# Kernel optimization log

Measured on AMD Instinct MI355X. Metric: run time of the kernel, lower is better.

## Reference

```python
import jax, jax.numpy as jnp
import numpy as np

B, T, H = 32, 2048, 1024

def setup_inputs() -> dict:
    key = jax.random.key(0)
    ks = jax.random.split(key, 8)
    s = 1.0 / np.sqrt(H)
    return {
        "query": jax.random.normal(ks[0], (B, H), dtype=jnp.float32),
        "values": jax.random.normal(ks[1], (B, T, H), dtype=jnp.float32),
        "Wq": jax.random.uniform(ks[2], (H, H), jnp.float32, -s, s),
        "bq": jax.random.uniform(ks[3], (H,), jnp.float32, -s, s),
        "Wv": jax.random.uniform(ks[4], (H, H), jnp.float32, -s, s),
        "bv": jax.random.uniform(ks[5], (H,), jnp.float32, -s, s),
        "Vw": jax.random.uniform(ks[6], (1, H), jnp.float32, -s, s),
        "Vb": jax.random.uniform(ks[7], (1,), jnp.float32, -s, s),
    }

def reference(query, values, Wq, bq, Wv, bv, Vw, Vb):
    # q_proj: [B,1,H], v_proj: [B,T,H]
    q_proj = (query @ Wq.T + bq)[:, None, :]
    v_proj = jnp.einsum('bth,oh->bto', values, Wv) + bv
    # score: [B,T,1] = tanh(...) @ Vw.T + Vb
    score = jnp.einsum('bth,oh->bto', jnp.tanh(q_proj + v_proj), Vw) + Vb
    attention_weights = jax.nn.softmax(score, axis=1)  # over time
    context_vector = jnp.sum(attention_weights * values, axis=1)  # [B,H]
    return (context_vector, attention_weights)
```

## Files before the change

### kernel.cpp

```cpp
#include <hip/hip_runtime.h>

#define BATCH 32
#define TT    2048
#define HH    1024
#define MTOT  (BATCH * TT)

typedef unsigned short ushort_t;
typedef short sh8 __attribute__((ext_vector_type(8)));
typedef float f4 __attribute__((ext_vector_type(4)));
typedef unsigned short us8 __attribute__((ext_vector_type(8)));

__device__ __forceinline__ ushort_t f2bf(float f) {
    unsigned u = __float_as_uint(f);
    u = (u + 0x7fffu + ((u >> 16) & 1u)) >> 16;
    return (ushort_t)u;
}
__device__ __forceinline__ float bf2f(ushort_t h) {
    return __uint_as_float(((unsigned)h) << 16);
}
__device__ __forceinline__ float fast_tanh(float x) {
    float e = __expf(2.0f * x);
    return 1.0f - 2.0f * __builtin_amdgcn_rcpf(e + 1.0f);
}

__device__ __forceinline__ void glds16(const void* g, void* l) {
    __builtin_amdgcn_global_load_lds(
        (const __attribute__((address_space(1))) void*)g,
        (__attribute__((address_space(3))) void*)l, 16, 0, 0);
}

__global__ void cvt_bf16_k(const float* __restrict__ in, ushort_t* __restrict__ out, long n) {
    long i = ((long)blockIdx.x * blockDim.x + threadIdx.x) * 8;
    if (i + 8 > n) return;
    float4 a = *(const float4*)(in + i);
    float4 b = *(const float4*)(in + i + 4);
    us8 o;
    o[0]=f2bf(a.x); o[1]=f2bf(a.y); o[2]=f2bf(a.z); o[3]=f2bf(a.w);
    o[4]=f2bf(b.x); o[5]=f2bf(b.y); o[6]=f2bf(b.z); o[7]=f2bf(b.w);
    *(us8*)(out + i) = o;
}

__global__ void qproj_k(const float* __restrict__ query, const float* __restrict__ Wq,
                        const float* __restrict__ bq, const float* __restrict__ bv,
                        float* __restrict__ qp) {
    int o = blockIdx.x, tid = threadIdx.x;
    float4 w4 = *(const float4*)(Wq + (long)o * HH + tid * 4);
    __shared__ float sm[BATCH][4];
    int wid = tid >> 6, lane = tid & 63;
    for (int b = 0; b < BATCH; ++b) {
        float4 q4 = *(const float4*)(query + (long)b * HH + tid * 4);
        float p = q4.x*w4.x + q4.y*w4.y + q4.z*w4.z + q4.w*w4.w;
        #pragma unroll
        for (int m = 1; m < 64; m <<= 1) p += __shfl_xor(p, m);
        if (lane == 0) sm[b][wid] = p;
    }
    __syncthreads();
    if (tid < BATCH) {
        float s = sm[tid][0] + sm[tid][1] + sm[tid][2] + sm[tid][3] + bq[o] + bv[o];
        qp[(long)tid * HH + o] = s;
    }
}


#define PBAR()  __builtin_amdgcn_s_barrier()
#define LGKM0() asm volatile("s_waitcnt lgkmcnt(0)" ::: "memory")
#define VMW(n)  asm volatile("s_waitcnt vmcnt(" #n ")" ::: "memory")
#define PRIO(p) __builtin_amdgcn_s_setprio(p)

__device__ __forceinline__ void stage_half(const ushort_t* __restrict__ gbase,
                                           long row0, int kb,
                                           char* ldsbase, int h, int w8, int lane) {
    #pragma unroll
    for (int c = 0; c < 2; ++c) {
        int r  = h * 128 + c * 64 + w8 + (lane >> 3);
        int sg = (lane & 7) ^ (r & 7);
        glds16(gbase + (row0 + r) * (long)HH + kb + sg * 8,
               ldsbase + (h * 128 + c * 64 + w8) * 128);
    }
}

#define READ_A(Lp, ibase)                                                        \
    { _Pragma("unroll") for (int i2_ = 0; i2_ < 4; ++i2_) {                      \
        int r_ = wr * 128 + ((ibase) + i2_) * 16 + l16;                          \
        _Pragma("unroll") for (int kq_ = 0; kq_ < 2; ++kq_)                      \
            af[i2_][kq_] = *(const sh8*)((Lp) + r_ * 128 +                       \
                                          ((((kq_ * 4) + quad) ^ (r_ & 7)) * 16)); } }

#define READ_B(Lp, jbase)                                                        \
    { _Pragma("unroll") for (int j2_ = 0; j2_ < 2; ++j2_) {                      \
        int r_ = wc * 64 + ((jbase) + j2_) * 16 + l16;                           \
        _Pragma("unroll") for (int kq_ = 0; kq_ < 2; ++kq_)                      \
            bf[(jbase) + j2_][kq_] = *(const sh8*)((Lp) + r_ * 128 +             \
                                          ((((kq_ * 4) + quad) ^ (r_ & 7)) * 16)); } }

#define MFMA_Q(ibase, jbase)                                                     \
    { _Pragma("unroll") for (int kq_ = 0; kq_ < 2; ++kq_) {                      \
      _Pragma("unroll") for (int i2_ = 0; i2_ < 4; ++i2_) {                      \
      _Pragma("unroll") for (int j2_ = 0; j2_ < 2; ++j2_) {                      \
            acc[(ibase) + i2_][(jbase) + j2_] =                                  \
                __builtin_amdgcn_mfma_f32_16x16x32_bf16(                         \
                    af[i2_][kq_], bf[(jbase) + j2_][kq_],                        \
                    acc[(ibase) + i2_][(jbase) + j2_], 0, 0, 0); } } } }

__global__ __launch_bounds__(512, 2) void score_gemm_k(
    const ushort_t* __restrict__ A, const ushort_t* __restrict__ Bw,
    const float* __restrict__ qp, const float* __restrict__ Vw,
    float* __restrict__ score)
{
    __shared__ ushort_t As[2][256 * 64];
    __shared__ ushort_t Bs[2][256 * 64];
    const int tid  = threadIdx.x;
    const int w    = tid >> 6, lane = tid & 63;
    const int quad = lane >> 4, l16 = lane & 15;
    const int wr   = w >> 2, wc = w & 3;
    const int w8   = w << 3;

    int bx   = blockIdx.x;
    int wgid = (bx & 7) * 128 + (bx >> 3);
    int mt   = wgid >> 2, nt = wgid & 3;
    const long m0 = (long)mt * 256;
    const long n0 = (long)nt * 256;

    char* As0 = (char*)&As[0][0];
    char* As1 = (char*)&As[1][0];
    char* Bs0 = (char*)&Bs[0][0];
    char* Bs1 = (char*)&Bs[1][0];

    f4  acc[8][4] = {};
    sh8 af[4][2], bf[4][2];

    stage_half(A,  m0, 0,  As0, 0, w8, lane);
    stage_half(A,  m0, 0,  As0, 1, w8, lane);
    stage_half(Bw, n0, 0,  Bs0, 0, w8, lane);
    stage_half(Bw, n0, 0,  Bs0, 1, w8, lane);
    stage_half(Bw, n0, 64, Bs1, 0, w8, lane);
    stage_half(Bw, n0, 64, Bs1, 1, w8, lane);
    VMW(4); PBAR();

    for (int it = 0; it < 7; ++it) {
        const int kb1 = (2 * it + 1) * 64;
        const int kb2 = (2 * it + 2) * 64;
        const int kb3 = (2 * it + 3) * 64;
        READ_A(As0, 0); READ_B(Bs0, 0);
        stage_half(A, m0, kb1, As1, 0, w8, lane);
        PBAR(); LGKM0(); PRIO(1); MFMA_Q(0, 0); PRIO(0); PBAR();
        READ_B(Bs0, 2);
        stage_half(A, m0, kb1, As1, 1, w8, lane);
        PBAR(); LGKM0(); PRIO(1); MFMA_Q(0, 2); PRIO(0); PBAR();
        READ_A(As0, 4);
        stage_half(Bw, n0, kb2, Bs0, 0, w8, lane);
        PBAR(); LGKM0(); PRIO(1); MFMA_Q(4, 2); PRIO(0); PBAR();
        stage_half(Bw, n0, kb2, Bs0, 1, w8, lane);
        VMW(4); PBAR(); PRIO(1); MFMA_Q(4, 0); PRIO(0); PBAR();
        READ_A(As1, 0); READ_B(Bs1, 0);
        stage_half(A, m0, kb2, As0, 0, w8, lane);
        PBAR(); LGKM0(); PRIO(1); MFMA_Q(0, 0); PRIO(0); PBAR();
        READ_B(Bs1, 2);
        stage_half(A, m0, kb2, As0, 1, w8, lane);
        PBAR(); LGKM0(); PRIO(1); MFMA_Q(0, 2); PRIO(0); PBAR();
        READ_A(As1, 4);
        stage_half(Bw, n0, kb3, Bs1, 0, w8, lane);
        PBAR(); LGKM0(); PRIO(1); MFMA_Q(4, 2); PRIO(0); PBAR();
        stage_half(Bw, n0, kb3, Bs1, 1, w8, lane);
        VMW(4); PBAR(); PRIO(1); MFMA_Q(4, 0); PRIO(0); PBAR();
    }
    {
        const int kb1 = 15 * 64;
        READ_A(As0, 0); READ_B(Bs0, 0);
        stage_half(A, m0, kb1, As1, 0, w8, lane);
        PBAR(); LGKM0(); PRIO(1); MFMA_Q(0, 0); PRIO(0); PBAR();
        READ_B(Bs0, 2);
        stage_half(A, m0, kb1, As1, 1, w8, lane);
        PBAR(); LGKM0(); PRIO(1); MFMA_Q(0, 2); PRIO(0); PBAR();
        READ_A(As0, 4);
        PBAR(); LGKM0(); PRIO(1); MFMA_Q(4, 2); PRIO(0); PBAR();
        VMW(0); PBAR(); PRIO(1); MFMA_Q(4, 0); PRIO(0); PBAR();
        READ_A(As1, 0); READ_B(Bs1, 0);
        PBAR(); LGKM0(); PRIO(1); MFMA_Q(0, 0); PRIO(0); PBAR();
        READ_B(Bs1, 2);
        PBAR(); LGKM0(); PRIO(1); MFMA_Q(0, 2); PRIO(0); PBAR();
        READ_A(As1, 4);
        PBAR(); LGKM0(); PRIO(1); MFMA_Q(4, 2); MFMA_Q(4, 0); PRIO(0);
    }

    int bidx = (int)(m0 >> 11);
    const float* qpb = qp + (long)bidx * HH;
    float qv[4], vw[4];
    #pragma unroll
    for (int j = 0; j < 4; ++j) {
        int cg = (int)n0 + wc * 64 + j * 16 + l16;
        qv[j] = qpb[cg];
        vw[j] = Vw[cg];
    }
    #pragma unroll
    for (int i = 0; i < 8; ++i) {
        #pragma unroll
        for (int r = 0; r < 4; ++r) {
            float sum = 0.0f;
            #pragma unroll
            for (int j = 0; j < 4; ++j) {
                float xv = acc[i][j][r] + qv[j];
                sum += fast_tanh(xv) * vw[j];
            }
            sum += __shfl_xor(sum, 1);
            sum += __shfl_xor(sum, 2);
            sum += __shfl_xor(sum, 4);
            sum += __shfl_xor(sum, 8);
            if (l16 == 0) {
                atomicAdd(score + m0 + wr * 128 + i * 16 + quad * 4 + r, sum);
            }
        }
    }
}

__global__ void softmax_k(const float* __restrict__ sc, float* __restrict__ w) {
    int b = blockIdx.x, tid = threadIdx.x;
    const float* s = sc + (long)b * TT;
    float v[8];
    float4 a0 = *(const float4*)(s + tid * 8);
    float4 a1 = *(const float4*)(s + tid * 8 + 4);
    v[0]=a0.x; v[1]=a0.y; v[2]=a0.z; v[3]=a0.w;
    v[4]=a1.x; v[5]=a1.y; v[6]=a1.z; v[7]=a1.w;
    float mx = v[0];
    #pragma unroll
    for (int i = 1; i < 8; ++i) mx = fmaxf(mx, v[i]);
    #pragma unroll
    for (int m = 1; m < 64; m <<= 1) mx = fmaxf(mx, __shfl_xor(mx, m));
    __shared__ float smx[4], ssum[4];
    int wid = tid >> 6;
    if ((tid & 63) == 0) smx[wid] = mx;
    __syncthreads();
    mx = fmaxf(fmaxf(smx[0], smx[1]), fmaxf(smx[2], smx[3]));
    float sum = 0.0f;
    #pragma unroll
    for (int i = 0; i < 8; ++i) { v[i] = __expf(v[i] - mx); sum += v[i]; }
    #pragma unroll
    for (int m = 1; m < 64; m <<= 1) sum += __shfl_xor(sum, m);
    if ((tid & 63) == 0) ssum[wid] = sum;
    __syncthreads();
    sum = ssum[0] + ssum[1] + ssum[2] + ssum[3];
    float inv = 1.0f / sum;
    float4 o0 = make_float4(v[0]*inv, v[1]*inv, v[2]*inv, v[3]*inv);
    float4 o1 = make_float4(v[4]*inv, v[5]*inv, v[6]*inv, v[7]*inv);
    *(float4*)(w + (long)b * TT + tid * 8)     = o0;
    *(float4*)(w + (long)b * TT + tid * 8 + 4) = o1;
}

__global__ void context_k2(const ushort_t* __restrict__ vb, const float* __restrict__ w,
                           float* __restrict__ partial) {
    int b = blockIdx.x, tc = blockIdx.y;
    int tid = threadIdx.x;
    int toff = tid >> 7;
    int hi   = tid & 127;
    int h    = hi * 8;
    __shared__ float sw[128];
    __shared__ float red[128][8];
    if (tid < 128) sw[tid] = w[(long)b * TT + tc * 128 + tid];
    __syncthreads();

    const ushort_t* base = vb + ((long)b * TT + tc * 128 + toff) * HH + h;
    float acc[8] = {0.f,0.f,0.f,0.f,0.f,0.f,0.f,0.f};
    #pragma unroll 8
    for (int it = 0; it < 64; ++it) {
        us8 v = *(const us8*)(base + (long)it * 2 * HH);
        float wt = sw[it * 2 + toff];
        #pragma unroll
        for (int e = 0; e < 8; ++e) acc[e] += wt * bf2f(v[e]);
    }
    if (toff == 1) {
        #pragma unroll
        for (int e = 0; e < 8; ++e) red[hi][e] = acc[e];
    }
    __syncthreads();
    if (toff == 0) {
        #pragma unroll
        for (int e = 0; e < 8; ++e) acc[e] += red[hi][e];
        float* p = partial + ((long)tc * 32 + b) * HH + h;
        *(float4*)(p)     = make_float4(acc[0], acc[1], acc[2], acc[3]);
        *(float4*)(p + 4) = make_float4(acc[4], acc[5], acc[6], acc[7]);
    }
}

__global__ void context_red_k(const float* __restrict__ partial, float* __restrict__ ctx) {
    int i = blockIdx.x * 256 + threadIdx.x;
    float s = 0.f;
    #pragma unroll
    for (int tc = 0; tc < 16; ++tc) s += partial[(long)tc * 32768 + i];
    ctx[i] = s;
}

extern "C" void kernel_launch(void* const* d_in, const int* in_sizes, int n_in,
                              void* d_out, int out_size, void* d_ws, size_t ws_size,
                              hipStream_t stream) {
    const float* query  = (const float*)d_in[0];
    const float* values = (const float*)d_in[1];
    const float* Wq     = (const float*)d_in[2];
    const float* bq     = (const float*)d_in[3];
    const float* Wv     = (const float*)d_in[4];
    const float* bv     = (const float*)d_in[5];
    const float* Vw     = (const float*)d_in[6];

    char* ws = (char*)d_ws;
    ushort_t* vb   = (ushort_t*)ws;
    ushort_t* wvb  = (ushort_t*)(ws + 134217728);
    float*    qp   = (float*)   (ws + 134217728 + 2097152);
    float*    scre = (float*)   (ws + 134217728 + 2097152 + 131072);
    float*    partial = (float*)wvb;

    float* ctx  = (float*)d_out;
    float* wout = (float*)d_out + BATCH * HH;

    hipMemsetAsync(scre, 0, (size_t)MTOT * 4, stream);

    cvt_bf16_k<<<(BATCH * TT * HH) / 2048, 256, 0, stream>>>(values, vb, (long)BATCH * TT * HH);
    cvt_bf16_k<<<(HH * HH) / 2048, 256, 0, stream>>>(Wv, wvb, (long)HH * HH);

    qproj_k<<<HH, 256, 0, stream>>>(query, Wq, bq, bv, qp);

    score_gemm_k<<<(MTOT / 256) * (HH / 256), 512, 0, stream>>>(vb, wvb, qp, Vw, scre);

    softmax_k<<<BATCH, 256, 0, stream>>>(scre, wout);

    context_k2<<<dim3(BATCH, 16), 256, 0, stream>>>(vb, wout, partial);
    context_red_k<<<(BATCH * HH) / 256, 256, 0, stream>>>(partial, ctx);
}
```

Baseline: 597.1 us.

## Merge Wv conversion, q-projection and score zeroing into one kernel; tune GEMM waits

The Wv bf16 conversion, the query projection and the zeroing of the score buffer are folded into a single prep kernel, which removes a memset and two separate kernel launches. In the score GEMM, the asm waitcnt statements lose their memory clobbers and sched_barrier fences are added around them. A partial lgkmcnt(8) wait is inserted before the barrier, and the LDS buffers are split into separate shared arrays. These edits aim to cut launch overhead and give the compiler freer instruction scheduling, at the risk of subtle ordering hazards now that the memory clobbers are gone.

Result: no change. 602.7 us (+0.9%).

```diff
diff --git a/kernel.cpp b/kernel.cpp
--- a/kernel.cpp
+++ b/kernel.cpp
@@ -40,10 +40,24 @@
     *(us8*)(out + i) = o;
 }
 
-__global__ void qproj_k(const float* __restrict__ query, const float* __restrict__ Wq,
-                        const float* __restrict__ bq, const float* __restrict__ bv,
-                        float* __restrict__ qp) {
-    int o = blockIdx.x, tid = threadIdx.x;
+__global__ void prep_k(const float* __restrict__ query, const float* __restrict__ Wq,
+                       const float* __restrict__ bq, const float* __restrict__ bv,
+                       float* __restrict__ qp,
+                       const float* __restrict__ Wv, ushort_t* __restrict__ wvb,
+                       float* __restrict__ scre) {
+    int bid = blockIdx.x, tid = threadIdx.x;
+    if (bid >= HH) {
+        long i = ((long)(bid - HH) * 256 + tid) * 8;
+        float4 a = *(const float4*)(Wv + i);
+        float4 b = *(const float4*)(Wv + i + 4);
+        us8 o;
+        o[0]=f2bf(a.x); o[1]=f2bf(a.y); o[2]=f2bf(a.z); o[3]=f2bf(a.w);
+        o[4]=f2bf(b.x); o[5]=f2bf(b.y); o[6]=f2bf(b.z); o[7]=f2bf(b.w);
+        *(us8*)(wvb + i) = o;
+        return;
+    }
+    int o = bid;
+    if (tid < 16) *(float4*)(scre + (long)o * 64 + tid * 4) = make_float4(0.f, 0.f, 0.f, 0.f);
     float4 w4 = *(const float4*)(Wq + (long)o * HH + tid * 4);
     __shared__ float sm[BATCH][4];
     int wid = tid >> 6, lane = tid & 63;
@@ -63,8 +77,10 @@
 
 
 #define PBAR()  __builtin_amdgcn_s_barrier()
-#define LGKM0() asm volatile("s_waitcnt lgkmcnt(0)" ::: "memory")
-#define VMW(n)  asm volatile("s_waitcnt vmcnt(" #n ")" ::: "memory")
+#define LGKM0() asm volatile("s_waitcnt lgkmcnt(0)")
+#define LGKM8() asm volatile("s_waitcnt lgkmcnt(8)")
+#define VMW(n)  asm volatile("s_waitcnt vmcnt(" #n ")")
+#define SCHB()  __builtin_amdgcn_sched_barrier(0)
 #define PRIO(p) __builtin_amdgcn_s_setprio(p)
 
 __device__ __forceinline__ void stage_half(const ushort_t* __restrict__ gbase,
@@ -107,8 +123,10 @@
     const float* __restrict__ qp, const float* __restrict__ Vw,
     float* __restrict__ score)
 {
-    __shared__ ushort_t As[2][256 * 64];
-    __shared__ ushort_t Bs[2][256 * 64];
+    __shared__ ushort_t As0s[256 * 64];
+    __shared__ ushort_t As1s[256 * 64];
+    __shared__ ushort_t Bs0s[256 * 64];
+    __shared__ ushort_t Bs1s[256 * 64];
     const int tid  = threadIdx.x;
     const int w    = tid >> 6, lane = tid & 63;
     const int quad = lane >> 4, l16 = lane & 15;
@@ -121,10 +139,10 @@
     const long m0 = (long)mt * 256;
     const long n0 = (long)nt * 256;
 
-    char* As0 = (char*)&As[0][0];
-    char* As1 = (char*)&As[1][0];
-    char* Bs0 = (char*)&Bs[0][0];
-    char* Bs1 = (char*)&Bs[1][0];
+    char* As0 = (char*)As0s;
+    char* As1 = (char*)As1s;
+    char* Bs0 = (char*)Bs0s;
+    char* Bs1 = (char*)Bs1s;
 
     f4  acc[8][4] = {};
     sh8 af[4][2], bf[4][2];
@@ -135,7 +153,7 @@
     stage_half(Bw, n0, 0,  Bs0, 1, w8, lane);
     stage_half(Bw, n0, 64, Bs1, 0, w8, lane);
     stage_half(Bw, n0, 64, Bs1, 1, w8, lane);
-    VMW(4); PBAR();
+    SCHB(); VMW(4); PBAR();
 
     for (int it = 0; it < 7; ++it) {
         const int kb1 = (2 * it + 1) * 64;
@@ -143,44 +161,47 @@
         const int kb3 = (2 * it + 3) * 64;
         READ_A(As0, 0); READ_B(Bs0, 0);
         stage_half(A, m0, kb1, As1, 0, w8, lane);
-        PBAR(); LGKM0(); PRIO(1); MFMA_Q(0, 0); PRIO(0); PBAR();
+        LGKM8();
+        PBAR(); LGKM0(); SCHB(); PRIO(1); MFMA_Q(0, 0); PRIO(0); PBAR();
         READ_B(Bs0, 2);
         stage_half(A, m0, kb1, As1, 1, w8, lane);
-        PBAR(); LGKM0(); PRIO(1); MFMA_Q(0, 2); PRIO(0); PBAR();
+        PBAR(); LGKM0(); SCHB(); PRIO(1); MFMA_Q(0, 2); PRIO(0); PBAR();
         READ_A(As0, 4);
         stage_half(Bw, n0, kb2, Bs0, 0, w8, lane);
-        PBAR(); LGKM0(); PRIO(1); MFMA_Q(4, 2); PRIO(0); PBAR();
+        PBAR(); LGKM0(); SCHB(); PRIO(1); MFMA_Q(4, 2); PRIO(0); PBAR();
         stage_half(Bw, n0, kb2, Bs0, 1, w8, lane);
-        VMW(4); PBAR(); PRIO(1); MFMA_Q(4, 0); PRIO(0); PBAR();
+        SCHB(); VMW(4); PBAR(); PRIO(1); MFMA_Q(4, 0); PRIO(0); PBAR();
         READ_A(As1, 0); READ_B(Bs1, 0);
         stage_half(A, m0, kb2, As0, 0, w8, lane);
-        PBAR(); LGKM0(); PRIO(1); MFMA_Q(0, 0); PRIO(0); PBAR();
+        LGKM8();
+        PBAR(); LGKM0(); SCHB(); PRIO(1); MFMA_Q(0, 0); PRIO(0); PBAR();
         READ_B(Bs1, 2);
         stage_half(A, m0, kb2, As0, 1, w8, lane);
-        PBAR(); LGKM0(); PRIO(1); MFMA_Q(0, 2); PRIO(0); PBAR();
+        PBAR(); LGKM0(); SCHB(); PRIO(1); MFMA_Q(0, 2); PRIO(0); PBAR();
         READ_A(As1, 4);
         stage_half(Bw, n0, kb3, Bs1, 0, w8, lane);
-        PBAR(); LGKM0(); PRIO(1); MFMA_Q(4, 2); PRIO(0); PBAR();
+        PBAR(); LGKM0(); SCHB(); PRIO(1); MFMA_Q(4, 2); PRIO(0); PBAR();
         stage_half(Bw, n0, kb3, Bs1, 1, w8, lane);
-        VMW(4); PBAR(); PRIO(1); MFMA_Q(4, 0); PRIO(0); PBAR();
+        SCHB(); VMW(4); PBAR(); PRIO(1); MFMA_Q(4, 0); PRIO(0); PBAR();
     }
     {
         const int kb1 = 15 * 64;
         READ_A(As0, 0); READ_B(Bs0, 0);
         stage_half(A, m0, kb1, As1, 0, w8, lane);
-        PBAR(); LGKM0(); PRIO(1); MFMA_Q(0, 0); PRIO(0); PBAR();
+        LGKM8();
+        PBAR(); LGKM0(); SCHB(); PRIO(1); MFMA_Q(0, 0); PRIO(0); PBAR();
         READ_B(Bs0, 2);
         stage_half(A, m0, kb1, As1, 1, w8, lane);
-        PBAR(); LGKM0(); PRIO(1); MFMA_Q(0, 2); PRIO(0); PBAR();
+        PBAR(); LGKM0(); SCHB(); PRIO(1); MFMA_Q(0, 2); PRIO(0); PBAR();
         READ_A(As0, 4);
-        PBAR(); LGKM0(); PRIO(1); MFMA_Q(4, 2); PRIO(0); PBAR();
-        VMW(0); PBAR(); PRIO(1); MFMA_Q(4, 0); PRIO(0); PBAR();
+        PBAR(); LGKM0(); SCHB(); PRIO(1); MFMA_Q(4, 2); PRIO(0); PBAR();
+        SCHB(); VMW(0); PBAR(); PRIO(1); MFMA_Q(4, 0); PRIO(0); PBAR();
         READ_A(As1, 0); READ_B(Bs1, 0);
-        PBAR(); LGKM0(); PRIO(1); MFMA_Q(0, 0); PRIO(0); PBAR();
+        PBAR(); LGKM0(); SCHB(); PRIO(1); MFMA_Q(0, 0); PRIO(0); PBAR();
         READ_B(Bs1, 2);
-        PBAR(); LGKM0(); PRIO(1); MFMA_Q(0, 2); PRIO(0); PBAR();
+        PBAR(); LGKM0(); SCHB(); PRIO(1); MFMA_Q(0, 2); PRIO(0); PBAR();
         READ_A(As1, 4);
-        PBAR(); LGKM0(); PRIO(1); MFMA_Q(4, 2); MFMA_Q(4, 0); PRIO(0);
+        PBAR(); LGKM0(); SCHB(); PRIO(1); MFMA_Q(4, 2); MFMA_Q(4, 0); PRIO(0);
     }
 
     int bidx = (int)(m0 >> 11);
@@ -310,12 +331,9 @@
     float* ctx  = (float*)d_out;
     float* wout = (float*)d_out + BATCH * HH;
 
-    hipMemsetAsync(scre, 0, (size_t)MTOT * 4, stream);
-
     cvt_bf16_k<<<(BATCH * TT * HH) / 2048, 256, 0, stream>>>(values, vb, (long)BATCH * TT * HH);
-    cvt_bf16_k<<<(HH * HH) / 2048, 256, 0, stream>>>(Wv, wvb, (long)HH * HH);
-
-    qproj_k<<<HH, 256, 0, stream>>>(query, Wq, bq, bv, qp);
+
+    prep_k<<<HH + (HH * HH) / 2048, 256, 0, stream>>>(query, Wq, bq, bv, qp, Wv, wvb, scre);
 
     score_gemm_k<<<(MTOT / 256) * (HH / 256), 512, 0, stream>>>(vb, wvb, qp, Vw, scre);
 
```
